# Optimization experiments

Measured on AMD Instinct MI355X. Metric: run time of the kernel, lower is better.

Reference implementation:

```python
import jax, jax.numpy as jnp
import numpy as np

B, DIM = 64, 131072


def setup_inputs() -> dict:
    key = jax.random.key(0)
    k1, k2, k3 = jax.random.split(key, 3)
    z = jax.random.normal(k1, (B, DIM), dtype=jnp.float32)
    trace_in = jax.random.normal(k2, (B, DIM), dtype=jnp.float32)
    ctrl = jax.random.normal(k3, (B, 3), dtype=jnp.float32)
    return {"z": z, "trace_in": trace_in, "ctrl": ctrl}


def reference(z, trace_in, ctrl):
    # gates: [B,1]
    store = jax.nn.sigmoid(ctrl[:, 0:1])
    retrieve = jax.nn.sigmoid(ctrl[:, 1:2])
    # clear gate only touches the internal buffer (no effect on outputs); omitted.

    # global max-abs normalization (single scalar, as in torch: z.abs().max())
    z_norm = z / (jnp.abs(z).max() + 1e-6)

    z_f = jnp.fft.fft(z_norm)          # [B,DIM] complex64
    trace_f = jnp.fft.fft(trace_in)    # [B,DIM] complex64
    new_trace_f = trace_f + z_f * store
    new_trace = jnp.fft.ifft(new_trace_f)
    read = jnp.fft.ifft(new_trace_f * jnp.conj(z_f)) * retrieve

    dummy_ptr = jnp.zeros((z.shape[0], 1), dtype=jnp.float32)
    return (read, new_trace, dummy_ptr, jnp.array(1.0, dtype=jnp.float32))
```

## Files before the change

### kernel.cpp

```cpp
#include <hip/hip_runtime.h>
#include <math.h>

#define NROW 64
#define DIM  131072

struct cf { float x, y; };
__device__ __forceinline__ cf cadd(cf a, cf b){ return {a.x+b.x, a.y+b.y}; }
__device__ __forceinline__ cf csub(cf a, cf b){ return {a.x-b.x, a.y-b.y}; }
__device__ __forceinline__ cf cmul(cf a, cf b){ return {a.x*b.x - a.y*b.y, a.x*b.y + a.y*b.x}; }
template<int SG> __device__ __forceinline__ cf muli(cf a){
  return (SG > 0) ? cf{-a.y, a.x} : cf{a.y, -a.x};
}
__device__ __forceinline__ float sigmoidf(float x){ return 1.0f/(1.0f + __expf(-x)); }

__device__ __forceinline__ void wsync(){
  __builtin_amdgcn_wave_barrier();
  asm volatile("" ::: "memory");
}

typedef float __attribute__((ext_vector_type(4))) fvec4;

template<int SG> __device__ __forceinline__ void fft4(cf&a0, cf&a1, cf&a2, cf&a3){
  cf e0=cadd(a0,a2), e1=csub(a0,a2), o0=cadd(a1,a3), o1=csub(a1,a3);
  cf w=muli<SG>(o1);
  a0=cadd(e0,o0); a2=csub(e0,o0); a1=cadd(e1,w); a3=csub(e1,w);
}

template<int SG> __device__ __forceinline__ void fft8(cf v[8]){
  cf e0=v[0], e1=v[2], e2=v[4], e3=v[6];
  cf o0=v[1], o1=v[3], o2=v[5], o3=v[7];
  fft4<SG>(e0,e1,e2,e3); fft4<SG>(o0,o1,o2,o3);
  const float R=0.70710678118654752f;
  cf w1=cmul(o1, cf{R, (float)SG*R});
  cf w2=muli<SG>(o2);
  cf w3=cmul(o3, cf{-R, (float)SG*R});
  v[0]=cadd(e0,o0); v[4]=csub(e0,o0);
  v[1]=cadd(e1,w1); v[5]=csub(e1,w1);
  v[2]=cadd(e2,w2); v[6]=csub(e2,w2);
  v[3]=cadd(e3,w3); v[7]=csub(e3,w3);
}

template<int SG> __device__ __forceinline__ void fft16(cf v[16]){
  cf e[8], o[8];
  #pragma unroll
  for(int i=0;i<8;i++){ e[i]=v[2*i]; o[i]=v[2*i+1]; }
  fft8<SG>(e); fft8<SG>(o);
  const float C[8]={1.f,0.92387953251128674f,0.70710678118654752f,0.38268343236508977f,
                    0.f,-0.38268343236508977f,-0.70710678118654752f,-0.92387953251128674f};
  const float S[8]={0.f,0.38268343236508977f,0.70710678118654752f,0.92387953251128674f,
                    1.f,0.92387953251128674f,0.70710678118654752f,0.38268343236508977f};
  #pragma unroll
  for(int k=0;k<8;k++){
    cf w=cmul(o[k], cf{C[k], (float)SG*S[k]});
    v[k]=cadd(e[k],w); v[k+8]=csub(e[k],w);
  }
}

__global__ void k0_tail(float* __restrict__ dout, int cplx){
  int t = threadIdx.x;
  size_t base = (size_t)2*NROW*DIM*cplx;
  if(t < NROW) dout[base + t] = 0.f;
  else if(t == NROW) dout[base + NROW] = 1.0f;
}

__global__ __launch_bounds__(256) void k1_maxabs(const float* __restrict__ z, unsigned* __restrict__ dst){
  __shared__ float red[256];
  size_t i0 = (size_t)blockIdx.x*blockDim.x + threadIdx.x;
  size_t stride = (size_t)gridDim.x*blockDim.x;
  const float4* z4 = (const float4*)z;
  size_t n4 = (size_t)NROW*DIM/4;
  float m = 0.f;
  for(size_t i=i0;i<n4;i+=stride){
    float4 v=z4[i];
    m = fmaxf(m, fmaxf(fmaxf(fabsf(v.x),fabsf(v.y)), fmaxf(fabsf(v.z),fabsf(v.w))));
  }
  red[threadIdx.x]=m; __syncthreads();
  #pragma unroll
  for(int s=128;s>0;s>>=1){
    if(threadIdx.x<(unsigned)s) red[threadIdx.x]=fmaxf(red[threadIdx.x],red[threadIdx.x+s]);
    __syncthreads();
  }
  if(threadIdx.x==0) atomicMax(dst, __float_as_uint(red[0]));
}

__global__ __launch_bounds__(256) void k2_fwd1(
    const float* __restrict__ z, const float* __restrict__ tr,
    const float* __restrict__ ctrl, const unsigned* __restrict__ maxbits,
    float2* __restrict__ Bws, float* __restrict__ out_nt, int cplx)
{
  __shared__ float reb[4384], imb[4384];
  __shared__ float twc[256], tws[256];
  int t = threadIdx.x;
  int b = blockIdx.x >> 5;
  int n1b = (blockIdx.x & 31) << 4;
  {
    float sv, cv;
    __sincosf(-0.0245436926061703f * (float)t, &sv, &cv);
    twc[t]=cv; tws[t]=sv;
  }
  float s = 1.0f/(__uint_as_float(*maxbits) + 1e-6f);
  float gs = sigmoidf(ctrl[b*3+0]);
  float cc = gs*s;
  const float4* zr4 = (const float4*)(z  + (size_t)b*DIM);
  const float4* tr4 = (const float4*)(tr + (size_t)b*DIM);
  #pragma unroll
  for(int it=0; it<4; ++it){
    int e = t + 256*it;
    int n2 = e >> 2, j4 = e & 3;
    int fi = n2*128 + (n1b>>2) + j4;
    float4 zv = zr4[fi];
    float4 tv = tr4[fi];
    int lb = n2*17 + j4*4;
    reb[lb+0]=zv.x; reb[lb+1]=zv.y; reb[lb+2]=zv.z; reb[lb+3]=zv.w;
    imb[lb+0]=tv.x; imb[lb+1]=tv.y; imb[lb+2]=tv.z; imb[lb+3]=tv.w;
    float n0 = fmaf(cc, zv.x, tv.x);
    float n1v= fmaf(cc, zv.y, tv.y);
    float n2v= fmaf(cc, zv.z, tv.z);
    float n3 = fmaf(cc, zv.w, tv.w);
    size_t n = (size_t)n2*512 + n1b + j4*4;
    size_t oidx = (size_t)b*DIM + n;
    if(cplx == 2){
      fvec4 a  = {n0, 0.f, n1v, 0.f};
      fvec4 bq = {n2v, 0.f, n3, 0.f};
      fvec4* op = (fvec4*)((float2*)out_nt + oidx);
      __builtin_nontemporal_store(a,  op);
      __builtin_nontemporal_store(bq, op+1);
    } else {
      out_nt[oidx+0]=n0; out_nt[oidx+1]=n1v; out_nt[oidx+2]=n2v; out_nt[oidx+3]=n3;
    }
  }
  __syncthreads();
  int f = t & 15, p = t >> 4;
  cf v[16];
  #pragma unroll
  for(int q=0;q<16;q++){ int n2=q*16+p; v[q].x=reb[n2*17+f]; v[q].y=imb[n2*17+f]; }
  fft16<-1>(v);
  #pragma unroll
  for(int kq=1;kq<16;kq++){ int tt=(p*kq)&255; v[kq]=cmul(v[kq], cf{twc[tt], tws[tt]}); }
  __syncthreads();
  #pragma unroll
  for(int kq=0;kq<16;kq++){ reb[f*274 + kq*17 + p]=v[kq].x; imb[f*274 + kq*17 + p]=v[kq].y; }
  __syncthreads();
  #pragma unroll
  for(int pp=0;pp<16;pp++){ v[pp].x=reb[f*274 + p*17 + pp]; v[pp].y=imb[f*274 + p*17 + pp]; }
  fft16<-1>(v);
  int nn1 = n1b + f;
  cf w, st;
  {
    float sv, cv;
    __sincosf(-4.793689960382698e-05f * (float)(nn1*p), &sv, &cv);
    w = {cv, sv};
    __sincosf(-4.793689960382698e-05f * 16.f * (float)nn1, &sv, &cv);
    st = {cv, sv};
  }
  #pragma unroll
  for(int kp=0;kp<16;kp++){
    int k2 = kp*16 + p;
    cf r = cmul(v[kp], w);
    Bws[((size_t)b<<17) + (size_t)k2*512 + nn1] = make_float2(r.x, r.y);
    w = cmul(w, st);
  }
}

template<int SG>
__device__ __forceinline__ void fft512_wave(
    float* Cre, float* Cim, int lane, const float* twc, const float* tws)
{
  cf v[8];
  int kQ = lane>>3, pp = lane&7;
  #pragma unroll
  for(int q=0;q<8;q++){ v[q].x=Cre[q*64+lane]; v[q].y=Cim[q*64+lane]; }
  fft8<SG>(v);
  #pragma unroll
  for(int kq=1;kq<8;kq++){
    int tt=(lane*kq)&511; int ti=tt&255; float sg=(tt&256)?-1.f:1.f;
    v[kq]=cmul(v[kq], cf{sg*twc[ti], (float)SG*sg*tws[ti]});
  }
  wsync();
  #pragma unroll
  for(int kq=0;kq<8;kq++){ Cre[lane*9+kq]=v[kq].x; Cim[lane*9+kq]=v[kq].y; }
  wsync();
  #pragma unroll
  for(int q=0;q<8;q++){ int idx=(q*8+pp)*9+kQ; v[q].x=Cre[idx]; v[q].y=Cim[idx]; }
  fft8<SG>(v);
  #pragma unroll
  for(int kq=1;kq<8;kq++){
    int tt=(pp*kq*8)&511; int ti=tt&255; float sg=(tt&256)?-1.f:1.f;
    v[kq]=cmul(v[kq], cf{sg*twc[ti], (float)SG*sg*tws[ti]});
  }
  wsync();
  #pragma unroll
  for(int kq=0;kq<8;kq++){ Cre[pp*73+kq*9+kQ]=v[kq].x; Cim[pp*73+kq*9+kQ]=v[kq].y; }
  wsync();
  #pragma unroll
  for(int p2=0;p2<8;p2++){ int idx=p2*73 + kQ*9 + pp; v[p2].x=Cre[idx]; v[p2].y=Cim[idx]; }
  fft8<SG>(v);
  wsync();
  #pragma unroll
  for(int kp=0;kp<8;kp++){ int k=kp*64 + kQ*8 + pp; Cre[k]=v[kp].x; Cim[k]=v[kp].y; }
  wsync();
}

__global__ __launch_bounds__(128) void k3_mid(
    float2* __restrict__ Bws, const float* __restrict__ ctrl,
    const unsigned* __restrict__ maxbits)
{
  __shared__ float Cbuf[2][1168];
  __shared__ float twc[256], tws[256];
  int t = threadIdx.x;
  int b  = blockIdx.x >> 7;
  int pr = blockIdx.x & 127;
  int cA = (pr==0) ? 0   : pr;
  int cB = (pr==0) ? 128 : 256-pr;
  int col = t >> 6, lane = t & 63;
  int myc = col ? cB : cA;
  for(int i=t;i<256;i+=128){
    float sv,cv; __sincosf(0.0122718463030851f*(float)i, &sv, &cv);
    twc[i]=cv; tws[i]=sv;
  }
  float s = 1.0f/(__uint_as_float(*maxbits)+1e-6f);
  float gs = sigmoidf(ctrl[b*3+0]);
  float alpha = sigmoidf(ctrl[b*3+1]) * (1.0f/(float)DIM);
  float* Cre = Cbuf[col]; float* Cim = Cre + 584;
  float2* colp = Bws + ((size_t)b<<17) + ((size_t)myc<<9);
  const float4* colp4 = (const float4*)colp;
  #pragma unroll
  for(int r=0;r<4;r++){
    float4 q = colp4[lane + 64*r];
    int j = 2*(lane + 64*r);
    Cre[j]=q.x;   Cim[j]=q.y;
    Cre[j+1]=q.z; Cim[j+1]=q.w;
  }
  __syncthreads();
  fft512_wave<-1>(Cre, Cim, lane, twc, tws);
  __syncthreads();
  const float* Pre = (pr==0) ? Cre : Cbuf[1-col];
  const float* Pim = Pre + 584;
  cf pv[8];
  #pragma unroll
  for(int rr=0;rr<8;rr++){
    int k1  = lane + 64*rr;
    int k1p = (myc==0) ? ((512-k1)&511) : (511-k1);
    float cr = Cre[k1], ci = Cim[k1];
    float qr = Pre[k1p], qi = -Pim[k1p];
    float zur = 0.5f*(cr+qr), zui = 0.5f*(ci+qi);
    float dr = cr-qr, di = ci-qi;
    float tfr = 0.5f*di, tfi = -0.5f*dr;
    float szr = s*zur, szi = s*zui;
    float ntr = fmaf(gs, szr, tfr), nti = fmaf(gs, szi, tfi);
    pv[rr].x = (ntr*szr + nti*szi)*alpha;
    pv[rr].y = (nti*szr - ntr*szi)*alpha;
  }
  __syncthreads();
  #pragma unroll
  for(int rr=0;rr<8;rr++){
    int k1 = lane + 64*rr;
    Cre[k1]=pv[rr].x; Cim[k1]=pv[rr].y;
  }
  wsync();
  fft512_wave<1>(Cre, Cim, lane, twc, tws);
  cf w, st;
  {
    float sv,cv;
    __sincosf(4.793689960382698e-05f * (float)(lane*myc), &sv, &cv);
    w = {cv, sv};
    __sincosf(4.793689960382698e-05f * 64.f * (float)myc, &sv, &cv);
    st = {cv, sv};
  }
  #pragma unroll
  for(int rr=0;rr<8;rr++){
    int m1 = lane + 64*rr;
    cf r2 = cmul(cf{Cre[m1],Cim[m1]}, w);
    colp[m1] = make_float2(r2.x, r2.y);
    w = cmul(w, st);
  }
}

__global__ __launch_bounds__(256) void k4_inv2(
    const float2* __restrict__ Qws, float* __restrict__ dout, int cplx)
{
  __shared__ float reb[4384], imb[4384];
  __shared__ float twc[256], tws[256];
  int t = threadIdx.x;
  int b = blockIdx.x >> 5;
  int m1b = (blockIdx.x & 31) << 4;
  {
    float sv, cv;
    __sincosf(0.0245436926061703f * (float)t, &sv, &cv);
    twc[t]=cv; tws[t]=sv;
  }
  const float4* Qp = (const float4*)(Qws + ((size_t)b<<17));
  #pragma unroll
  for(int it=0; it<8; ++it){
    int e = t + 256*it;
    int k2 = e >> 3, j = e & 7;
    float4 q = Qp[k2*256 + (m1b>>1) + j];
    int lb = k2*17 + 2*j;
    reb[lb+0]=q.x; imb[lb+0]=q.y;
    reb[lb+1]=q.z; imb[lb+1]=q.w;
  }
  __syncthreads();
  int f = t & 15, p = t >> 4;
  cf v[16];
  #pragma unroll
  for(int q=0;q<16;q++){ int k2=q*16+p; v[q].x=reb[k2*17+f]; v[q].y=imb[k2*17+f]; }
  fft16<1>(v);
  #pragma unroll
  for(int kq=1;kq<16;kq++){ int tt=(p*kq)&255; v[kq]=cmul(v[kq], cf{twc[tt], tws[tt]}); }
  __syncthreads();
  #pragma unroll
  for(int kq=0;kq<16;kq++){ reb[f*274+kq*17+p]=v[kq].x; imb[f*274+kq*17+p]=v[kq].y; }
  __syncthreads();
  #pragma unroll
  for(int pp=0;pp<16;pp++){ v[pp].x=reb[f*274+p*17+pp]; v[pp].y=imb[f*274+p*17+pp]; }
  fft16<1>(v);
  #pragma unroll
  for(int kp=0;kp<16;kp++){
    int m2 = kp*16 + p;
    size_t n = (size_t)(m1b + f) + (size_t)512*m2;
    size_t oidx = (size_t)b*DIM + n;
    if(cplx==2){
      ((float2*)dout)[oidx] = make_float2(v[kp].x, 0.f);
    }
    else dout[oidx] = v[kp].x;
  }
}

extern "C" void kernel_launch(void* const* d_in, const int* in_sizes, int n_in,
                              void* d_out, int out_size, void* d_ws, size_t ws_size,
                              hipStream_t stream)
{
  (void)in_sizes; (void)n_in; (void)ws_size;
  const float* z    = (const float*)d_in[0];
  const float* tr   = (const float*)d_in[1];
  const float* ctrl = (const float*)d_in[2];
  float* dout = (float*)d_out;
  int cplx = (out_size > 20000000) ? 2 : 1;
  unsigned* maxbits = (unsigned*)d_ws;
  float2* Bws = (float2*)((char*)d_ws + 256);

  hipMemsetAsync(d_ws, 0, 4, stream);
  hipLaunchKernelGGL(k0_tail,  dim3(1),    dim3(128), 0, stream, dout, cplx);
  hipLaunchKernelGGL(k1_maxabs,dim3(1024), dim3(256), 0, stream, z, maxbits);
  hipLaunchKernelGGL(k2_fwd1,  dim3(2048), dim3(256), 0, stream,
                     z, tr, ctrl, maxbits, Bws, dout + (size_t)NROW*DIM*cplx, cplx);
  hipLaunchKernelGGL(k3_mid,   dim3(8192), dim3(128), 0, stream, Bws, ctrl, maxbits);
  hipLaunchKernelGGL(k4_inv2,  dim3(2048), dim3(256), 0, stream, Bws, dout, cplx);
}
```

Before: 215.9 us.

## Pack two real-output rows into one complex inverse FFT

The middle kernel now handles two batch rows per block and combines their spectra as A + iB. A single inverse FFT then serves both rows, and the last kernel writes the real part to one row and the imaginary part to the next. This relies on each row's inverse result being real. It halves the inverse-FFT compute and the workspace writes and reads in the final stages. In exchange each k3 block does two forward column FFTs, which uses more registers and lowers parallelism.

```diff
diff --git a/kernel.cpp b/kernel.cpp
--- a/kernel.cpp
+++ b/kernel.cpp
@@ -208,8 +208,9 @@
   __shared__ float Cbuf[2][1168];
   __shared__ float twc[256], tws[256];
   int t = threadIdx.x;
-  int b  = blockIdx.x >> 7;
+  int bp = blockIdx.x >> 7;
   int pr = blockIdx.x & 127;
+  int b0 = bp*2, b1 = b0+1;
   int cA = (pr==0) ? 0   : pr;
   int cB = (pr==0) ? 128 : 256-pr;
   int col = t >> 6, lane = t & 63;
@@ -219,24 +220,30 @@
     twc[i]=cv; tws[i]=sv;
   }
   float s = 1.0f/(__uint_as_float(*maxbits)+1e-6f);
-  float gs = sigmoidf(ctrl[b*3+0]);
-  float alpha = sigmoidf(ctrl[b*3+1]) * (1.0f/(float)DIM);
+  float gs0 = sigmoidf(ctrl[b0*3+0]);
+  float al0 = sigmoidf(ctrl[b0*3+1]) * (1.0f/(float)DIM);
+  float gs1 = sigmoidf(ctrl[b1*3+0]);
+  float al1 = sigmoidf(ctrl[b1*3+1]) * (1.0f/(float)DIM);
   float* Cre = Cbuf[col]; float* Cim = Cre + 584;
-  float2* colp = Bws + ((size_t)b<<17) + ((size_t)myc<<9);
-  const float4* colp4 = (const float4*)colp;
-  #pragma unroll
-  for(int r=0;r<4;r++){
-    float4 q = colp4[lane + 64*r];
-    int j = 2*(lane + 64*r);
-    Cre[j]=q.x;   Cim[j]=q.y;
-    Cre[j+1]=q.z; Cim[j+1]=q.w;
-  }
-  __syncthreads();
-  fft512_wave<-1>(Cre, Cim, lane, twc, tws);
-  __syncthreads();
   const float* Pre = (pr==0) ? Cre : Cbuf[1-col];
   const float* Pim = Pre + 584;
-  cf pv[8];
+  float2* colp0 = Bws + ((size_t)b0<<17) + ((size_t)myc<<9);
+  float2* colp1 = Bws + ((size_t)b1<<17) + ((size_t)myc<<9);
+  cf pv0[8], pv1[8];
+
+  {
+    const float4* c4 = (const float4*)colp0;
+    #pragma unroll
+    for(int r=0;r<4;r++){
+      float4 q = c4[lane + 64*r];
+      int j = 2*(lane + 64*r);
+      Cre[j]=q.x;   Cim[j]=q.y;
+      Cre[j+1]=q.z; Cim[j+1]=q.w;
+    }
+  }
+  __syncthreads();
+  fft512_wave<-1>(Cre, Cim, lane, twc, tws);
+  __syncthreads();
   #pragma unroll
   for(int rr=0;rr<8;rr++){
     int k1  = lane + 64*rr;
@@ -247,15 +254,46 @@
     float dr = cr-qr, di = ci-qi;
     float tfr = 0.5f*di, tfi = -0.5f*dr;
     float szr = s*zur, szi = s*zui;
-    float ntr = fmaf(gs, szr, tfr), nti = fmaf(gs, szi, tfi);
-    pv[rr].x = (ntr*szr + nti*szi)*alpha;
-    pv[rr].y = (nti*szr - ntr*szi)*alpha;
-  }
-  __syncthreads();
+    float ntr = fmaf(gs0, szr, tfr), nti = fmaf(gs0, szi, tfi);
+    pv0[rr].x = (ntr*szr + nti*szi)*al0;
+    pv0[rr].y = (nti*szr - ntr*szi)*al0;
+  }
+  __syncthreads();
+
+  {
+    const float4* c4 = (const float4*)colp1;
+    #pragma unroll
+    for(int r=0;r<4;r++){
+      float4 q = c4[lane + 64*r];
+      int j = 2*(lane + 64*r);
+      Cre[j]=q.x;   Cim[j]=q.y;
+      Cre[j+1]=q.z; Cim[j+1]=q.w;
+    }
+  }
+  wsync();
+  fft512_wave<-1>(Cre, Cim, lane, twc, tws);
+  __syncthreads();
+  #pragma unroll
+  for(int rr=0;rr<8;rr++){
+    int k1  = lane + 64*rr;
+    int k1p = (myc==0) ? ((512-k1)&511) : (511-k1);
+    float cr = Cre[k1], ci = Cim[k1];
+    float qr = Pre[k1p], qi = -Pim[k1p];
+    float zur = 0.5f*(cr+qr), zui = 0.5f*(ci+qi);
+    float dr = cr-qr, di = ci-qi;
+    float tfr = 0.5f*di, tfi = -0.5f*dr;
+    float szr = s*zur, szi = s*zui;
+    float ntr = fmaf(gs1, szr, tfr), nti = fmaf(gs1, szi, tfi);
+    pv1[rr].x = (ntr*szr + nti*szi)*al1;
+    pv1[rr].y = (nti*szr - ntr*szi)*al1;
+  }
+  __syncthreads();
+
   #pragma unroll
   for(int rr=0;rr<8;rr++){
     int k1 = lane + 64*rr;
-    Cre[k1]=pv[rr].x; Cim[k1]=pv[rr].y;
+    Cre[k1] = pv0[rr].x - pv1[rr].y;
+    Cim[k1] = pv0[rr].y + pv1[rr].x;
   }
   wsync();
   fft512_wave<1>(Cre, Cim, lane, twc, tws);
@@ -271,7 +309,7 @@
   for(int rr=0;rr<8;rr++){
     int m1 = lane + 64*rr;
     cf r2 = cmul(cf{Cre[m1],Cim[m1]}, w);
-    colp[m1] = make_float2(r2.x, r2.y);
+    colp0[m1] = make_float2(r2.x, r2.y);
     w = cmul(w, st);
   }
 }
@@ -282,14 +320,15 @@
   __shared__ float reb[4384], imb[4384];
   __shared__ float twc[256], tws[256];
   int t = threadIdx.x;
-  int b = blockIdx.x >> 5;
+  int bp = blockIdx.x >> 5;
   int m1b = (blockIdx.x & 31) << 4;
+  int b0 = bp*2;
   {
     float sv, cv;
     __sincosf(0.0245436926061703f * (float)t, &sv, &cv);
     twc[t]=cv; tws[t]=sv;
   }
-  const float4* Qp = (const float4*)(Qws + ((size_t)b<<17));
+  const float4* Qp = (const float4*)(Qws + ((size_t)b0<<17));
   #pragma unroll
   for(int it=0; it<8; ++it){
     int e = t + 256*it;
@@ -318,11 +357,14 @@
   for(int kp=0;kp<16;kp++){
     int m2 = kp*16 + p;
     size_t n = (size_t)(m1b + f) + (size_t)512*m2;
-    size_t oidx = (size_t)b*DIM + n;
+    size_t o0 = (size_t)b0*DIM + n;
     if(cplx==2){
-      ((float2*)dout)[oidx] = make_float2(v[kp].x, 0.f);
+      ((float2*)dout)[o0]       = make_float2(v[kp].x, 0.f);
+      ((float2*)dout)[o0 + DIM] = make_float2(v[kp].y, 0.f);
+    } else {
+      dout[o0]       = v[kp].x;
+      dout[o0 + DIM] = v[kp].y;
     }
-    else dout[oidx] = v[kp].x;
   }
 }
 
@@ -344,6 +386,6 @@
   hipLaunchKernelGGL(k1_maxabs,dim3(1024), dim3(256), 0, stream, z, maxbits);
   hipLaunchKernelGGL(k2_fwd1,  dim3(2048), dim3(256), 0, stream,
                      z, tr, ctrl, maxbits, Bws, dout + (size_t)NROW*DIM*cplx, cplx);
-  hipLaunchKernelGGL(k3_mid,   dim3(8192), dim3(128), 0, stream, Bws, ctrl, maxbits);
-  hipLaunchKernelGGL(k4_inv2,  dim3(2048), dim3(256), 0, stream, Bws, dout, cplx);
-}
+  hipLaunchKernelGGL(k3_mid,   dim3(4096), dim3(128), 0, stream, Bws, ctrl, maxbits);
+  hipLaunchKernelGGL(k4_inv2,  dim3(1024), dim3(256), 0, stream, Bws, dout, cplx);
+}
```

Result: faster. 203.5 us (-5.7%).
